# Optimization experiments

Measured on AMD Instinct MI355X. Metric: run time of the kernel, lower is better.

The kernel has to match this reference:

```python
import jax, jax.numpy as jnp
import numpy as np

H = 512   # hidden_size
E = 256   # embedding_size
V = 32000 # vocab_size
L = 1024  # max_length (encoder seq len)
B = 64    # batch


def setup_inputs() -> dict:
    key = jax.random.key(0)
    ks = jax.random.split(key, 18)
    n = lambda i, shape, s=0.05: (jax.random.normal(ks[i], shape, dtype=jnp.float32) * s)
    return {
        "input": jax.random.randint(ks[0], (B, 1), 0, V),
        "last_output_context": n(1, (1, B, H), 1.0),
        "last_hidden": n(2, (1, B, H), 1.0),
        "last_cell_state": n(3, (1, B, H), 1.0),
        "encoder_outputs": n(4, (L, B, H), 1.0),
        "emb": n(5, (V, E)),
        "W_ih": n(6, (4 * H, E + H)),
        "W_hh": n(7, (4 * H, H)),
        "b_ih": n(8, (4 * H,)),
        "b_hh": n(9, (4 * H,)),
        "W_attn": n(10, (H, 2 * H)),
        "b_attn": n(11, (H,)),
        "beta": n(12, (H, 1), 1.0),
        "W_oc": n(13, (H, 2 * H)),
        "b_oc": n(14, (H,)),
        "W_out": n(15, (V, H)),
        "b_out": n(16, (V,)),
    }


def reference(input, last_output_context, last_hidden, last_cell_state,
              encoder_outputs, emb, W_ih, W_hh, b_ih, b_hh,
              W_attn, b_attn, beta, W_oc, b_oc, W_out, b_out):
    # embedding lookup: (B,1) -> (B,E)  (permute(1,0,2) then squeeze step dim)
    tok = emb[input[:, 0]]                                   # (B, E)
    x = jnp.concatenate([tok, last_output_context[0]], axis=1)  # (B, E+H)
    # single-step LSTM (PyTorch gate order i, f, g, o)
    gates = x @ W_ih.T + last_hidden[0] @ W_hh.T + b_ih + b_hh  # (B, 4H)
    i_g, f_g, g_g, o_g = jnp.split(gates, 4, axis=1)
    i_g = jax.nn.sigmoid(i_g)
    f_g = jax.nn.sigmoid(f_g)
    g_g = jnp.tanh(g_g)
    o_g = jax.nn.sigmoid(o_g)
    c = f_g * last_cell_state[0] + i_g * g_g                  # (B, H)
    h = o_g * jnp.tanh(c)                                     # (B, H) == rnn_output
    # additive attention, vectorized over the seq_len loop
    h_tiled = jnp.broadcast_to(h[None], (L, B, H))
    cat = jnp.concatenate([h_tiled, encoder_outputs], axis=-1)  # (L, B, 2H)
    energy = jnp.tanh(cat @ W_attn.T + b_attn) @ beta           # (L, B, 1)
    attn_w = jax.nn.softmax(energy[..., 0], axis=0)             # (L, B) softmax over seq
    # context = bmm(attn_weights, encoder_outputs)
    context = jnp.einsum('lb,lbh->bh', attn_w, encoder_outputs)  # (B, H)
    co = jnp.tanh(jnp.concatenate([h, context], axis=1) @ W_oc.T + b_oc)  # (B, H)
    output = jax.nn.log_softmax(co @ W_out.T + b_out, axis=1)    # (B, V)
    return output, co[None], h[None], c[None]
```

## Files before the change

### kernel.cpp

```cpp
#include <hip/hip_runtime.h>
#include <hip/hip_bf16.h>
#include <cstddef>

#define H   512
#define E   256
#define V   32000
#define L   1024
#define B   64
#define KX  768
#define M_TOT 65536

typedef __attribute__((ext_vector_type(8))) short short8v;
typedef __attribute__((ext_vector_type(4))) float f32x4;

union fu32 { float f; unsigned u; };

__device__ __forceinline__ void split2(float x, unsigned short& h, unsigned short& l) {
    fu32 v; v.f = x;
    h = (unsigned short)(v.u >> 16);
    fu32 hf; hf.u = v.u & 0xFFFF0000u;
    fu32 rv; rv.f = x - hf.f;
    l = (unsigned short)(rv.u >> 16);
}

__global__ __launch_bounds__(256) void k_split_w(const float* __restrict__ W_attn,
                                                 unsigned short* __restrict__ Wh,
                                                 unsigned short* __restrict__ Wl) {
    int e0 = blockIdx.x * 2048 + threadIdx.x * 8;
    int j = e0 >> 9, k = e0 & 511;
    const float* src = &W_attn[(size_t)j * (2 * H) + H + k];
    float4 x0 = *reinterpret_cast<const float4*>(src);
    float4 x1 = *reinterpret_cast<const float4*>(src + 4);
    float xs[8] = {x0.x, x0.y, x0.z, x0.w, x1.x, x1.y, x1.z, x1.w};
    union { short8v v; unsigned short u[8]; } hi, lo;
    #pragma unroll
    for (int i = 0; i < 8; ++i) split2(xs[i], hi.u[i], lo.u[i]);
    *reinterpret_cast<short8v*>(&Wh[e0]) = hi.v;
    *reinterpret_cast<short8v*>(&Wl[e0]) = lo.v;
}

__global__ __launch_bounds__(256) void k_build(const int* __restrict__ inp,
                                               const float* __restrict__ loc,
                                               const float* __restrict__ hprev,
                                               const float* __restrict__ emb,
                                               float* __restrict__ xprevT) {
    int gid = blockIdx.x * 256 + threadIdx.x;
    int k = gid >> 6, b = gid & 63;
    float v;
    if (k < 256)      v = emb[(size_t)inp[b] * E + k];
    else if (k < 768) v = loc[b * H + (k - 256)];
    else              v = hprev[b * H + (k - 768)];
    xprevT[gid] = v;
}

__global__ __launch_bounds__(256) void k_lstm(const float* __restrict__ W_ih,
                                              const float* __restrict__ W_hh,
                                              const float* __restrict__ b_ih,
                                              const float* __restrict__ b_hh,
                                              const float* __restrict__ xprevT,
                                              const float* __restrict__ cprev,
                                              float* __restrict__ h_out,
                                              float* __restrict__ c_out,
                                              float* __restrict__ hnewT) {
    int u = blockIdx.x;
    int w = threadIdx.x >> 6;
    int b = threadIdx.x & 63;
    int j = w * 512 + u;
    float a0 = 0.f, a1 = 0.f, a2 = 0.f, a3 = 0.f;
    const float* Wr = &W_ih[(size_t)j * KX];
    for (int k = 0; k < KX; k += 4) {
        float4 wv = *reinterpret_cast<const float4*>(&Wr[k]);
        a0 += wv.x * xprevT[(k + 0) * 64 + b];
        a1 += wv.y * xprevT[(k + 1) * 64 + b];
        a2 += wv.z * xprevT[(k + 2) * 64 + b];
        a3 += wv.w * xprevT[(k + 3) * 64 + b];
    }
    const float* Wr2 = &W_hh[(size_t)j * H];
    const float* hT = &xprevT[KX * 64];
    for (int k = 0; k < H; k += 4) {
        float4 wv = *reinterpret_cast<const float4*>(&Wr2[k]);
        a0 += wv.x * hT[(k + 0) * 64 + b];
        a1 += wv.y * hT[(k + 1) * 64 + b];
        a2 += wv.z * hT[(k + 2) * 64 + b];
        a3 += wv.w * hT[(k + 3) * 64 + b];
    }
    float acc = b_ih[j] + b_hh[j] + ((a0 + a1) + (a2 + a3));
    __shared__ float gs[4][64];
    gs[w][b] = acc;
    __syncthreads();
    if (threadIdx.x < 64) {
        float ig = 1.f / (1.f + __expf(-gs[0][b]));
        float fg = 1.f / (1.f + __expf(-gs[1][b]));
        float gg = tanhf(gs[2][b]);
        float og = 1.f / (1.f + __expf(-gs[3][b]));
        float c = fg * cprev[b * H + u] + ig * gg;
        float h = og * tanhf(c);
        c_out[b * H + u] = c;
        h_out[b * H + u] = h;
        hnewT[u * 64 + b] = h;
    }
}

__global__ __launch_bounds__(256) void k_hw(const float* __restrict__ W_attn,
                                            const float* __restrict__ b_attn,
                                            const float* __restrict__ hT,
                                            float* __restrict__ hW_jb) {
    int j = blockIdx.x * 4 + (threadIdx.x >> 6);
    int b = threadIdx.x & 63;
    float a0 = 0.f, a1 = 0.f, a2 = 0.f, a3 = 0.f;
    const float* Wr = &W_attn[(size_t)j * (2 * H)];
    for (int k = 0; k < H; k += 4) {
        float4 wv = *reinterpret_cast<const float4*>(&Wr[k]);
        a0 += wv.x * hT[(k + 0) * 64 + b];
        a1 += wv.y * hT[(k + 1) * 64 + b];
        a2 += wv.z * hT[(k + 2) * 64 + b];
        a3 += wv.w * hT[(k + 3) * 64 + b];
    }
    hW_jb[j * 64 + b] = b_attn[j] + ((a0 + a1) + (a2 + a3));
}

#define BKE 32
#define PITCH 40

__global__ __launch_bounds__(256, 3) void k_energy_v3(
        const float* __restrict__ enc,
        const unsigned short* __restrict__ Wh,
        const unsigned short* __restrict__ Wl,
        const float* __restrict__ hW,
        const float* __restrict__ beta,
        float* __restrict__ partial_e) {
    __shared__ unsigned short Ah[128 * PITCH];
    __shared__ unsigned short Al[128 * PITCH];
    __shared__ unsigned short Bh[128 * PITCH];
    __shared__ unsigned short Bl[128 * PITCH];
    __shared__ float red[2][128];

    const int tid  = threadIdx.x;
    const int lane = tid & 63;
    const int wave = tid >> 6;
    const int wm = wave >> 1;
    const int wn = wave & 1;
    const int mt = blockIdx.x >> 2;
    const int jt = blockIdx.x & 3;
    const int m0 = mt * 128;
    const int j0 = jt * 128;

    const int srow = tid >> 2;
    const int skc  = tid & 3;

    float4 ra0[2], ra1[2];
    short8v rb_h[2], rb_l[2];
    #pragma unroll
    for (int p = 0; p < 2; ++p) {
        int row = p * 64 + srow;
        const float* asrc = &enc[(size_t)(m0 + row) * H + skc * 8];
        ra0[p] = *reinterpret_cast<const float4*>(asrc);
        ra1[p] = *reinterpret_cast<const float4*>(asrc + 4);
        size_t bo = (size_t)(j0 + row) * H + skc * 8;
        rb_h[p] = *reinterpret_cast<const short8v*>(&Wh[bo]);
        rb_l[p] = *reinterpret_cast<const short8v*>(&Wl[bo]);
    }

    f32x4 acc[4][4];
    #pragma unroll
    for (int i = 0; i < 4; ++i)
        #pragma unroll
        for (int j = 0; j < 4; ++j) acc[i][j] = (f32x4){0.f, 0.f, 0.f, 0.f};

    for (int k0 = 0; k0 < H; k0 += BKE) {
        __syncthreads();
        #pragma unroll
        for (int p = 0; p < 2; ++p) {
            float xs[8] = {ra0[p].x, ra0[p].y, ra0[p].z, ra0[p].w,
                           ra1[p].x, ra1[p].y, ra1[p].z, ra1[p].w};
            union { short8v v; unsigned short u[8]; } hi, lo;
            #pragma unroll
            for (int i = 0; i < 8; ++i) split2(xs[i], hi.u[i], lo.u[i]);
            int off = (p * 64 + srow) * PITCH + skc * 8;
            *reinterpret_cast<short8v*>(&Ah[off]) = hi.v;
            *reinterpret_cast<short8v*>(&Al[off]) = lo.v;
            *reinterpret_cast<short8v*>(&Bh[off]) = rb_h[p];
            *reinterpret_cast<short8v*>(&Bl[off]) = rb_l[p];
        }
        __syncthreads();
        if (k0 + BKE < H) {
            int kn = k0 + BKE;
            #pragma unroll
            for (int p = 0; p < 2; ++p) {
                int row = p * 64 + srow;
                const float* asrc = &enc[(size_t)(m0 + row) * H + kn + skc * 8];
                ra0[p] = *reinterpret_cast<const float4*>(asrc);
                ra1[p] = *reinterpret_cast<const float4*>(asrc + 4);
                size_t bo = (size_t)(j0 + row) * H + kn + skc * 8;
                rb_h[p] = *reinterpret_cast<const short8v*>(&Wh[bo]);
                rb_l[p] = *reinterpret_cast<const short8v*>(&Wl[bo]);
            }
        }
        const int fr = lane & 15;
        const int kb = (lane >> 4) * 8;
        short8v a_h[4], a_l[4], b_h[4], b_l[4];
        #pragma unroll
        for (int mf = 0; mf < 4; ++mf) {
            int off = (wm * 64 + mf * 16 + fr) * PITCH + kb;
            a_h[mf] = *reinterpret_cast<const short8v*>(&Ah[off]);
            a_l[mf] = *reinterpret_cast<const short8v*>(&Al[off]);
        }
        #pragma unroll
        for (int nf = 0; nf < 4; ++nf) {
            int off = (wn * 64 + nf * 16 + fr) * PITCH + kb;
            b_h[nf] = *reinterpret_cast<const short8v*>(&Bh[off]);
            b_l[nf] = *reinterpret_cast<const short8v*>(&Bl[off]);
        }
        #pragma unroll
        for (int mf = 0; mf < 4; ++mf)
            #pragma unroll
            for (int nf = 0; nf < 4; ++nf) {
                acc[mf][nf] = __builtin_amdgcn_mfma_f32_16x16x32_bf16(
                    a_h[mf], b_h[nf], acc[mf][nf], 0, 0, 0);
                acc[mf][nf] = __builtin_amdgcn_mfma_f32_16x16x32_bf16(
                    a_h[mf], b_l[nf], acc[mf][nf], 0, 0, 0);
                acc[mf][nf] = __builtin_amdgcn_mfma_f32_16x16x32_bf16(
                    a_l[mf], b_h[nf], acc[mf][nf], 0, 0, 0);
            }
    }
    float psum[4][4];
    #pragma unroll
    for (int i = 0; i < 4; ++i)
        #pragma unroll
        for (int r = 0; r < 4; ++r) psum[i][r] = 0.f;
    #pragma unroll
    for (int nf = 0; nf < 4; ++nf) {
        int jj = j0 + wn * 64 + nf * 16 + (lane & 15);
        float bet = beta[jj];
        #pragma unroll
        for (int mf = 0; mf < 4; ++mf) {
            int b_base = (wm * 64 + mf * 16 + (lane >> 4) * 4) & 63;
            float4 hw4 = *reinterpret_cast<const float4*>(&hW[jj * 64 + b_base]);
            float hwv[4] = {hw4.x, hw4.y, hw4.z, hw4.w};
            #pragma unroll
            for (int r = 0; r < 4; ++r) {
                float e = acc[mf][nf][r] + hwv[r];
                float ex = __expf(2.f * e);
                psum[mf][r] += bet * (1.f - 2.f / (ex + 1.f));
            }
        }
    }
    #pragma unroll
    for (int mf = 0; mf < 4; ++mf)
        #pragma unroll
        for (int r = 0; r < 4; ++r) {
            float v = psum[mf][r];
            v += __shfl_xor(v, 1);
            v += __shfl_xor(v, 2);
            v += __shfl_xor(v, 4);
            v += __shfl_xor(v, 8);
            psum[mf][r] = v;
        }
    __syncthreads();
    if ((lane & 15) == 0) {
        #pragma unroll
        for (int mf = 0; mf < 4; ++mf)
            #pragma unroll
            for (int r = 0; r < 4; ++r)
                red[wn][wm * 64 + mf * 16 + (lane >> 4) * 4 + r] = psum[mf][r];
    }
    __syncthreads();
    if (tid < 128)
        partial_e[(size_t)jt * M_TOT + m0 + tid] = red[0][tid] + red[1][tid];
}

__global__ __launch_bounds__(256) void k_softmax_l(const float* __restrict__ partial_e,
                                                   float* __restrict__ attn_w) {
    int b = blockIdx.x;
    int tid = threadIdx.x;
    float el[4];
    float m = -1e30f;
    #pragma unroll
    for (int i = 0; i < 4; ++i) {
        int l = i * 256 + tid;
        float e = 0.f;
        #pragma unroll
        for (int nb = 0; nb < 4; ++nb)
            e += partial_e[(size_t)nb * M_TOT + l * 64 + b];
        el[i] = e;
        m = fmaxf(m, e);
    }
    #pragma unroll
    for (int s = 1; s < 64; s <<= 1) m = fmaxf(m, __shfl_xor(m, s));
    __shared__ float redm[4];
    if ((tid & 63) == 0) redm[tid >> 6] = m;
    __syncthreads();
    m = fmaxf(fmaxf(redm[0], redm[1]), fmaxf(redm[2], redm[3]));
    float s = 0.f;
    #pragma unroll
    for (int i = 0; i < 4; ++i) { el[i] = __expf(el[i] - m); s += el[i]; }
    #pragma unroll
    for (int sh = 1; sh < 64; sh <<= 1) s += __shfl_xor(s, sh);
    __shared__ float reds[4];
    if ((tid & 63) == 0) reds[tid >> 6] = s;
    __syncthreads();
    s = reds[0] + reds[1] + reds[2] + reds[3];
    float inv = 1.f / s;
    #pragma unroll
    for (int i = 0; i < 4; ++i)
        attn_w[(i * 256 + tid) * 64 + b] = el[i] * inv;
}

__global__ __launch_bounds__(256) void k_ctx_part(const float* __restrict__ attn_w,
                                                  const float* __restrict__ enc,
                                                  float* __restrict__ ctx_part) {
    int chunk = blockIdx.x, b = blockIdx.y;
    int h = threadIdx.x * 2;
    float2 acc = {0.f, 0.f};
    for (int i = 0; i < 32; ++i) {
        int l = chunk * 32 + i;
        float w = attn_w[l * 64 + b];
        float2 e2 = *reinterpret_cast<const float2*>(
            &enc[((size_t)l * 64 + b) * H + h]);
        acc.x += w * e2.x;
        acc.y += w * e2.y;
    }
    *reinterpret_cast<float2*>(&ctx_part[((size_t)(chunk * 64 + b)) * H + h]) = acc;
}

__global__ __launch_bounds__(256) void k_ctx_reduce(const float* __restrict__ ctx_part,
                                                    float* __restrict__ ctxT) {
    int gid = blockIdx.x * 256 + threadIdx.x;
    int b = gid >> 9, h = gid & 511;
    float s = 0.f;
    for (int c = 0; c < 32; ++c)
        s += ctx_part[((size_t)(c * 64 + b)) * H + h];
    ctxT[h * 64 + b] = s;
}

__global__ __launch_bounds__(256) void k_co(const float* __restrict__ W_oc,
                                            const float* __restrict__ b_oc,
                                            const float* __restrict__ hT,
                                            const float* __restrict__ ctxT,
                                            float* __restrict__ co_out) {
    int j = blockIdx.x * 4 + (threadIdx.x >> 6);
    int b = threadIdx.x & 63;
    float a0 = 0.f, a1 = 0.f, a2 = 0.f, a3 = 0.f;
    const float* Wr = &W_oc[(size_t)j * (2 * H)];
    for (int k = 0; k < H; k += 4) {
        float4 wv = *reinterpret_cast<const float4*>(&Wr[k]);
        a0 += wv.x * hT[(k + 0) * 64 + b];
        a1 += wv.y * hT[(k + 1) * 64 + b];
        a2 += wv.z * hT[(k + 2) * 64 + b];
        a3 += wv.w * hT[(k + 3) * 64 + b];
    }
    const float* Wr2 = Wr + H;
    for (int k = 0; k < H; k += 4) {
        float4 wv = *reinterpret_cast<const float4*>(&Wr2[k]);
        a0 += wv.x * ctxT[(k + 0) * 64 + b];
        a1 += wv.y * ctxT[(k + 1) * 64 + b];
        a2 += wv.z * ctxT[(k + 2) * 64 + b];
        a3 += wv.w * ctxT[(k + 3) * 64 + b];
    }
    co_out[b * H + j] = tanhf(b_oc[j] + ((a0 + a1) + (a2 + a3)));
}

__global__ __launch_bounds__(256) void k_logits_mfma(const float* __restrict__ co,
                                                     const float* __restrict__ W_out,
                                                     const float* __restrict__ b_out,
                                                     float* __restrict__ logits) {
    __shared__ unsigned short Ah[64 * PITCH];
    __shared__ unsigned short Al[64 * PITCH];
    __shared__ unsigned short Bh[64 * PITCH];
    __shared__ unsigned short Bl[64 * PITCH];

    const int tid  = threadIdx.x;
    const int lane = tid & 63;
    const int wave = tid >> 6;
    const int wm = wave >> 1;
    const int wn = wave & 1;
    const int j0 = blockIdx.x * 64;

    const int srow = tid >> 2;
    const int skc  = tid & 3;

    float4 ra0, ra1, rb0, rb1;
    {
        const float* as = &co[(size_t)srow * H + skc * 8];
        ra0 = *reinterpret_cast<const float4*>(as);
        ra1 = *reinterpret_cast<const float4*>(as + 4);
        const float* bs = &W_out[(size_t)(j0 + srow) * H + skc * 8];
        rb0 = *reinterpret_cast<const float4*>(bs);
        rb1 = *reinterpret_cast<const float4*>(bs + 4);
    }

    f32x4 acc[2][2];
    #pragma unroll
    for (int i = 0; i < 2; ++i)
        #pragma unroll
        for (int j = 0; j < 2; ++j) acc[i][j] = (f32x4){0.f, 0.f, 0.f, 0.f};

    for (int k0 = 0; k0 < H; k0 += BKE) {
        __syncthreads();
        {
            float xs[8] = {ra0.x, ra0.y, ra0.z, ra0.w, ra1.x, ra1.y, ra1.z, ra1.w};
            union { short8v v; unsigned short u[8]; } hi, lo;
            #pragma unroll
            for (int i = 0; i < 8; ++i) split2(xs[i], hi.u[i], lo.u[i]);
            int off = srow * PITCH + skc * 8;
            *reinterpret_cast<short8v*>(&Ah[off]) = hi.v;
            *reinterpret_cast<short8v*>(&Al[off]) = lo.v;
            float ys[8] = {rb0.x, rb0.y, rb0.z, rb0.w, rb1.x, rb1.y, rb1.z, rb1.w};
            union { short8v v; unsigned short u[8]; } hib, lob;
            #pragma unroll
            for (int i = 0; i < 8; ++i) split2(ys[i], hib.u[i], lob.u[i]);
            *reinterpret_cast<short8v*>(&Bh[off]) = hib.v;
            *reinterpret_cast<short8v*>(&Bl[off]) = lob.v;
        }
        __syncthreads();
        if (k0 + BKE < H) {
            int kn = k0 + BKE;
            const float* as = &co[(size_t)srow * H + kn + skc * 8];
            ra0 = *reinterpret_cast<const float4*>(as);
            ra1 = *reinterpret_cast<const float4*>(as + 4);
            const float* bs = &W_out[(size_t)(j0 + srow) * H + kn + skc * 8];
            rb0 = *reinterpret_cast<const float4*>(bs);
            rb1 = *reinterpret_cast<const float4*>(bs + 4);
        }
        const int fr = lane & 15;
        const int kb = (lane >> 4) * 8;
        short8v a_h[2], a_l[2], b_h[2], b_l[2];
        #pragma unroll
        for (int mf = 0; mf < 2; ++mf) {
            int off = (wm * 32 + mf * 16 + fr) * PITCH + kb;
            a_h[mf] = *reinterpret_cast<const short8v*>(&Ah[off]);
            a_l[mf] = *reinterpret_cast<const short8v*>(&Al[off]);
        }
        #pragma unroll
        for (int nf = 0; nf < 2; ++nf) {
            int off = (wn * 32 + nf * 16 + fr) * PITCH + kb;
            b_h[nf] = *reinterpret_cast<const short8v*>(&Bh[off]);
            b_l[nf] = *reinterpret_cast<const short8v*>(&Bl[off]);
        }
        #pragma unroll
        for (int mf = 0; mf < 2; ++mf)
            #pragma unroll
            for (int nf = 0; nf < 2; ++nf) {
                acc[mf][nf] = __builtin_amdgcn_mfma_f32_16x16x32_bf16(
                    a_h[mf], b_h[nf], acc[mf][nf], 0, 0, 0);
                acc[mf][nf] = __builtin_amdgcn_mfma_f32_16x16x32_bf16(
                    a_h[mf], b_l[nf], acc[mf][nf], 0, 0, 0);
                acc[mf][nf] = __builtin_amdgcn_mfma_f32_16x16x32_bf16(
                    a_l[mf], b_h[nf], acc[mf][nf], 0, 0, 0);
            }
    }
    #pragma unroll
    for (int nf = 0; nf < 2; ++nf) {
        int j = j0 + wn * 32 + nf * 16 + (lane & 15);
        float bo = b_out[j];
        #pragma unroll
        for (int mf = 0; mf < 2; ++mf) {
            int mbase = wm * 32 + mf * 16 + (lane >> 4) * 4;
            #pragma unroll
            for (int r = 0; r < 4; ++r)
                logits[(size_t)(mbase + r) * V + j] = acc[mf][nf][r] + bo;
        }
    }
}

__global__ __launch_bounds__(1024) void k_logsm(const float* __restrict__ logits,
                                                float* __restrict__ out) {
    int b = blockIdx.x;
    int tid = threadIdx.x;
    const float* row = &logits[(size_t)b * V];
    float m = -1e30f;
    for (int i = tid; i < V; i += 1024) m = fmaxf(m, row[i]);
    #pragma unroll
    for (int s = 1; s < 64; s <<= 1) m = fmaxf(m, __shfl_xor(m, s));
    __shared__ float redm[16];
    if ((tid & 63) == 0) redm[tid >> 6] = m;
    __syncthreads();
    m = redm[0];
    #pragma unroll
    for (int i = 1; i < 16; ++i) m = fmaxf(m, redm[i]);
    float s = 0.f;
    for (int i = tid; i < V; i += 1024) s += __expf(row[i] - m);
    #pragma unroll
    for (int sh = 1; sh < 64; sh <<= 1) s += __shfl_xor(s, sh);
    __shared__ float reds[16];
    if ((tid & 63) == 0) reds[tid >> 6] = s;
    __syncthreads();
    s = reds[0];
    #pragma unroll
    for (int i = 1; i < 16; ++i) s += reds[i];
    float lse = m + __logf(s);
    for (int i = tid; i < V; i += 1024)
        out[(size_t)b * V + i] = row[i] - lse;
}

extern "C" void kernel_launch(void* const* d_in, const int* in_sizes, int n_in,
                              void* d_out, int out_size, void* d_ws, size_t ws_size,
                              hipStream_t stream) {
    const int*   inp    = (const int*)  d_in[0];
    const float* loc    = (const float*)d_in[1];
    const float* hprev  = (const float*)d_in[2];
    const float* cprev  = (const float*)d_in[3];
    const float* enc    = (const float*)d_in[4];
    const float* emb    = (const float*)d_in[5];
    const float* W_ih   = (const float*)d_in[6];
    const float* W_hh   = (const float*)d_in[7];
    const float* b_ih   = (const float*)d_in[8];
    const float* b_hh   = (const float*)d_in[9];
    const float* W_attn = (const float*)d_in[10];
    const float* b_attn = (const float*)d_in[11];
    const float* beta   = (const float*)d_in[12];
    const float* W_oc   = (const float*)d_in[13];
    const float* b_oc   = (const float*)d_in[14];
    const float* W_out  = (const float*)d_in[15];
    const float* b_out  = (const float*)d_in[16];

    float* out = (float*)d_out;
    float* out_co = out + (size_t)B * V;
    float* out_h  = out_co + B * H;
    float* out_c  = out_h  + B * H;

    float* ws = (float*)d_ws;
    float* xprevT = ws;
    float* hnewT  = xprevT + 1280 * 64;
    float* hW     = hnewT  + H * 64;
    float* pe     = hW     + H * 64;
    float* attnw  = pe     + 4 * M_TOT;
    float* ctxp   = attnw  + M_TOT;
    float* ctxT   = ctxp   + 32 * 64 * H;
    float* logits = ctxT   + H * 64;
    float* ws_end = logits + (size_t)B * V;
    unsigned short* Wh = (unsigned short*)ws_end;
    unsigned short* Wl = Wh + H * H;

    k_split_w<<<128, 256, 0, stream>>>(W_attn, Wh, Wl);
    k_build <<<320, 256, 0, stream>>>(inp, loc, hprev, emb, xprevT);
    k_lstm  <<<512, 256, 0, stream>>>(W_ih, W_hh, b_ih, b_hh, xprevT, cprev,
                                      out_h, out_c, hnewT);
    k_hw    <<<128, 256, 0, stream>>>(W_attn, b_attn, hnewT, hW);
    k_energy_v3<<<2048, 256, 0, stream>>>(enc, Wh, Wl, hW, beta, pe);
    k_softmax_l<<<64, 256, 0, stream>>>(pe, attnw);
    k_ctx_part <<<dim3(32, 64), 256, 0, stream>>>(attnw, enc, ctxp);
    k_ctx_reduce<<<128, 256, 0, stream>>>(ctxp, ctxT);
    k_co    <<<128, 256, 0, stream>>>(W_oc, b_oc, hnewT, ctxT, out_co);
    k_logits_mfma<<<500, 256, 0, stream>>>(out_co, W_out, b_out, logits);
    k_logsm <<<64, 1024, 0, stream>>>(logits, out);
}
```

Measured before the change: 288.7 us.

## Switch energy and logits GEMMs to single-pass fp16 MFMA and split log-softmax

Replaces the three-MFMA bf16 hi/lo split emulation of fp32 in the attention-energy and output-logits GEMMs with a single fp16 MFMA per tile. This cuts MFMA work, halves LDS traffic and footprint, and lets the energy kernel target more blocks per CU. The log-softmax becomes a parallel three-stage partial max/sum, combine and vectorized write, and the context kernel switches to float4 loads. The cost is fp16 precision (about 11-bit mantissa, limited range) on the GEMMs, which may loosen accuracy against the fp32 reference.

```diff
diff --git a/kernel.cpp b/kernel.cpp
--- a/kernel.cpp
+++ b/kernel.cpp
@@ -10,33 +10,21 @@
 #define KX  768
 #define M_TOT 65536
 
-typedef __attribute__((ext_vector_type(8))) short short8v;
+typedef __attribute__((ext_vector_type(8))) _Float16 half8v;
 typedef __attribute__((ext_vector_type(4))) float f32x4;
 
-union fu32 { float f; unsigned u; };
-
-__device__ __forceinline__ void split2(float x, unsigned short& h, unsigned short& l) {
-    fu32 v; v.f = x;
-    h = (unsigned short)(v.u >> 16);
-    fu32 hf; hf.u = v.u & 0xFFFF0000u;
-    fu32 rv; rv.f = x - hf.f;
-    l = (unsigned short)(rv.u >> 16);
-}
-
-__global__ __launch_bounds__(256) void k_split_w(const float* __restrict__ W_attn,
-                                                 unsigned short* __restrict__ Wh,
-                                                 unsigned short* __restrict__ Wl) {
+__global__ __launch_bounds__(256) void k_conv_w(const float* __restrict__ W_attn,
+                                                unsigned short* __restrict__ Wf) {
     int e0 = blockIdx.x * 2048 + threadIdx.x * 8;
     int j = e0 >> 9, k = e0 & 511;
     const float* src = &W_attn[(size_t)j * (2 * H) + H + k];
     float4 x0 = *reinterpret_cast<const float4*>(src);
     float4 x1 = *reinterpret_cast<const float4*>(src + 4);
     float xs[8] = {x0.x, x0.y, x0.z, x0.w, x1.x, x1.y, x1.z, x1.w};
-    union { short8v v; unsigned short u[8]; } hi, lo;
-    #pragma unroll
-    for (int i = 0; i < 8; ++i) split2(xs[i], hi.u[i], lo.u[i]);
-    *reinterpret_cast<short8v*>(&Wh[e0]) = hi.v;
-    *reinterpret_cast<short8v*>(&Wl[e0]) = lo.v;
+    union { half8v v; _Float16 u[8]; } hv;
+    #pragma unroll
+    for (int i = 0; i < 8; ++i) hv.u[i] = (_Float16)xs[i];
+    *reinterpret_cast<half8v*>(&Wf[e0]) = hv.v;
 }
 
 __global__ __launch_bounds__(256) void k_build(const int* __restrict__ inp,
@@ -122,17 +110,14 @@
 #define BKE 32
 #define PITCH 40
 
-__global__ __launch_bounds__(256, 3) void k_energy_v3(
+__global__ __launch_bounds__(256, 4) void k_energy_v4(
         const float* __restrict__ enc,
-        const unsigned short* __restrict__ Wh,
-        const unsigned short* __restrict__ Wl,
+        const unsigned short* __restrict__ Wf,
         const float* __restrict__ hW,
         const float* __restrict__ beta,
         float* __restrict__ partial_e) {
     __shared__ unsigned short Ah[128 * PITCH];
-    __shared__ unsigned short Al[128 * PITCH];
     __shared__ unsigned short Bh[128 * PITCH];
-    __shared__ unsigned short Bl[128 * PITCH];
     __shared__ float red[2][128];
 
     const int tid  = threadIdx.x;
@@ -149,16 +134,14 @@
     const int skc  = tid & 3;
 
     float4 ra0[2], ra1[2];
-    short8v rb_h[2], rb_l[2];
+    half8v rb[2];
     #pragma unroll
     for (int p = 0; p < 2; ++p) {
         int row = p * 64 + srow;
         const float* asrc = &enc[(size_t)(m0 + row) * H + skc * 8];
         ra0[p] = *reinterpret_cast<const float4*>(asrc);
         ra1[p] = *reinterpret_cast<const float4*>(asrc + 4);
-        size_t bo = (size_t)(j0 + row) * H + skc * 8;
-        rb_h[p] = *reinterpret_cast<const short8v*>(&Wh[bo]);
-        rb_l[p] = *reinterpret_cast<const short8v*>(&Wl[bo]);
+        rb[p] = *reinterpret_cast<const half8v*>(&Wf[(size_t)(j0 + row) * H + skc * 8]);
     }
 
     f32x4 acc[4][4];
@@ -173,14 +156,12 @@
         for (int p = 0; p < 2; ++p) {
             float xs[8] = {ra0[p].x, ra0[p].y, ra0[p].z, ra0[p].w,
                            ra1[p].x, ra1[p].y, ra1[p].z, ra1[p].w};
-            union { short8v v; unsigned short u[8]; } hi, lo;
-            #pragma unroll
-            for (int i = 0; i < 8; ++i) split2(xs[i], hi.u[i], lo.u[i]);
+            union { half8v v; _Float16 u[8]; } hv;
+            #pragma unroll
+            for (int i = 0; i < 8; ++i) hv.u[i] = (_Float16)xs[i];
             int off = (p * 64 + srow) * PITCH + skc * 8;
-            *reinterpret_cast<short8v*>(&Ah[off]) = hi.v;
-            *reinterpret_cast<short8v*>(&Al[off]) = lo.v;
-            *reinterpret_cast<short8v*>(&Bh[off]) = rb_h[p];
-            *reinterpret_cast<short8v*>(&Bl[off]) = rb_l[p];
+            *reinterpret_cast<half8v*>(&Ah[off]) = hv.v;
+            *reinterpret_cast<half8v*>(&Bh[off]) = rb[p];
         }
         __syncthreads();
         if (k0 + BKE < H) {
@@ -191,37 +172,28 @@
                 const float* asrc = &enc[(size_t)(m0 + row) * H + kn + skc * 8];
                 ra0[p] = *reinterpret_cast<const float4*>(asrc);
                 ra1[p] = *reinterpret_cast<const float4*>(asrc + 4);
-                size_t bo = (size_t)(j0 + row) * H + kn + skc * 8;
-                rb_h[p] = *reinterpret_cast<const short8v*>(&Wh[bo]);
-                rb_l[p] = *reinterpret_cast<const short8v*>(&Wl[bo]);
+                rb[p] = *reinterpret_cast<const half8v*>(&Wf[(size_t)(j0 + row) * H + kn + skc * 8]);
             }
         }
         const int fr = lane & 15;
         const int kb = (lane >> 4) * 8;
-        short8v a_h[4], a_l[4], b_h[4], b_l[4];
+        half8v a_h[4], b_h[4];
         #pragma unroll
         for (int mf = 0; mf < 4; ++mf) {
             int off = (wm * 64 + mf * 16 + fr) * PITCH + kb;
-            a_h[mf] = *reinterpret_cast<const short8v*>(&Ah[off]);
-            a_l[mf] = *reinterpret_cast<const short8v*>(&Al[off]);
+            a_h[mf] = *reinterpret_cast<const half8v*>(&Ah[off]);
         }
         #pragma unroll
         for (int nf = 0; nf < 4; ++nf) {
             int off = (wn * 64 + nf * 16 + fr) * PITCH + kb;
-            b_h[nf] = *reinterpret_cast<const short8v*>(&Bh[off]);
-            b_l[nf] = *reinterpret_cast<const short8v*>(&Bl[off]);
+            b_h[nf] = *reinterpret_cast<const half8v*>(&Bh[off]);
         }
         #pragma unroll
         for (int mf = 0; mf < 4; ++mf)
             #pragma unroll
-            for (int nf = 0; nf < 4; ++nf) {
-                acc[mf][nf] = __builtin_amdgcn_mfma_f32_16x16x32_bf16(
+            for (int nf = 0; nf < 4; ++nf)
+                acc[mf][nf] = __builtin_amdgcn_mfma_f32_16x16x32_f16(
                     a_h[mf], b_h[nf], acc[mf][nf], 0, 0, 0);
-                acc[mf][nf] = __builtin_amdgcn_mfma_f32_16x16x32_bf16(
-                    a_h[mf], b_l[nf], acc[mf][nf], 0, 0, 0);
-                acc[mf][nf] = __builtin_amdgcn_mfma_f32_16x16x32_bf16(
-                    a_l[mf], b_h[nf], acc[mf][nf], 0, 0, 0);
-            }
     }
     float psum[4][4];
     #pragma unroll
@@ -306,21 +278,23 @@
         attn_w[(i * 256 + tid) * 64 + b] = el[i] * inv;
 }
 
-__global__ __launch_bounds__(256) void k_ctx_part(const float* __restrict__ attn_w,
+__global__ __launch_bounds__(128) void k_ctx_part(const float* __restrict__ attn_w,
                                                   const float* __restrict__ enc,
                                                   float* __restrict__ ctx_part) {
     int chunk = blockIdx.x, b = blockIdx.y;
-    int h = threadIdx.x * 2;
-    float2 acc = {0.f, 0.f};
+    int h = threadIdx.x * 4;
+    float4 acc = {0.f, 0.f, 0.f, 0.f};
     for (int i = 0; i < 32; ++i) {
         int l = chunk * 32 + i;
         float w = attn_w[l * 64 + b];
-        float2 e2 = *reinterpret_cast<const float2*>(
+        float4 e4 = *reinterpret_cast<const float4*>(
             &enc[((size_t)l * 64 + b) * H + h]);
-        acc.x += w * e2.x;
-        acc.y += w * e2.y;
-    }
-    *reinterpret_cast<float2*>(&ctx_part[((size_t)(chunk * 64 + b)) * H + h]) = acc;
+        acc.x += w * e4.x;
+        acc.y += w * e4.y;
+        acc.z += w * e4.z;
+        acc.w += w * e4.w;
+    }
+    *reinterpret_cast<float4*>(&ctx_part[((size_t)(chunk * 64 + b)) * H + h]) = acc;
 }
 
 __global__ __launch_bounds__(256) void k_ctx_reduce(const float* __restrict__ ctx_part,
@@ -360,14 +334,12 @@
     co_out[b * H + j] = tanhf(b_oc[j] + ((a0 + a1) + (a2 + a3)));
 }
 
-__global__ __launch_bounds__(256) void k_logits_mfma(const float* __restrict__ co,
-                                                     const float* __restrict__ W_out,
-                                                     const float* __restrict__ b_out,
-                                                     float* __restrict__ logits) {
+__global__ __launch_bounds__(256) void k_logits_v2(const float* __restrict__ co,
+                                                   const float* __restrict__ W_out,
+                                                   const float* __restrict__ b_out,
+                                                   float* __restrict__ logits) {
     __shared__ unsigned short Ah[64 * PITCH];
-    __shared__ unsigned short Al[64 * PITCH];
     __shared__ unsigned short Bh[64 * PITCH];
-    __shared__ unsigned short Bl[64 * PITCH];
 
     const int tid  = threadIdx.x;
     const int lane = tid & 63;
@@ -399,18 +371,16 @@
         __syncthreads();
         {
             float xs[8] = {ra0.x, ra0.y, ra0.z, ra0.w, ra1.x, ra1.y, ra1.z, ra1.w};
-            union { short8v v; unsigned short u[8]; } hi, lo;
-            #pragma unroll
-            for (int i = 0; i < 8; ++i) split2(xs[i], hi.u[i], lo.u[i]);
+            union { half8v v; _Float16 u[8]; } ha;
+            #pragma unroll
+            for (int i = 0; i < 8; ++i) ha.u[i] = (_Float16)xs[i];
+            float ys[8] = {rb0.x, rb0.y, rb0.z, rb0.w, rb1.x, rb1.y, rb1.z, rb1.w};
+            union { half8v v; _Float16 u[8]; } hb;
+            #pragma unroll
+            for (int i = 0; i < 8; ++i) hb.u[i] = (_Float16)ys[i];
             int off = srow * PITCH + skc * 8;
-            *reinterpret_cast<short8v*>(&Ah[off]) = hi.v;
-            *reinterpret_cast<short8v*>(&Al[off]) = lo.v;
-            float ys[8] = {rb0.x, rb0.y, rb0.z, rb0.w, rb1.x, rb1.y, rb1.z, rb1.w};
-            union { short8v v; unsigned short u[8]; } hib, lob;
-            #pragma unroll
-            for (int i = 0; i < 8; ++i) split2(ys[i], hib.u[i], lob.u[i]);
-            *reinterpret_cast<short8v*>(&Bh[off]) = hib.v;
-            *reinterpret_cast<short8v*>(&Bl[off]) = lob.v;
+            *reinterpret_cast<half8v*>(&Ah[off]) = ha.v;
+            *reinterpret_cast<half8v*>(&Bh[off]) = hb.v;
         }
         __syncthreads();
         if (k0 + BKE < H) {
@@ -424,30 +394,23 @@
         }
         const int fr = lane & 15;
         const int kb = (lane >> 4) * 8;
-        short8v a_h[2], a_l[2], b_h[2], b_l[2];
+        half8v a_h[2], b_h[2];
         #pragma unroll
         for (int mf = 0; mf < 2; ++mf) {
             int off = (wm * 32 + mf * 16 + fr) * PITCH + kb;
-            a_h[mf] = *reinterpret_cast<const short8v*>(&Ah[off]);
-            a_l[mf] = *reinterpret_cast<const short8v*>(&Al[off]);
+            a_h[mf] = *reinterpret_cast<const half8v*>(&Ah[off]);
         }
         #pragma unroll
         for (int nf = 0; nf < 2; ++nf) {
             int off = (wn * 32 + nf * 16 + fr) * PITCH + kb;
-            b_h[nf] = *reinterpret_cast<const short8v*>(&Bh[off]);
-            b_l[nf] = *reinterpret_cast<const short8v*>(&Bl[off]);
+            b_h[nf] = *reinterpret_cast<const half8v*>(&Bh[off]);
         }
         #pragma unroll
         for (int mf = 0; mf < 2; ++mf)
             #pragma unroll
-            for (int nf = 0; nf < 2; ++nf) {
-                acc[mf][nf] = __builtin_amdgcn_mfma_f32_16x16x32_bf16(
+            for (int nf = 0; nf < 2; ++nf)
+                acc[mf][nf] = __builtin_amdgcn_mfma_f32_16x16x32_f16(
                     a_h[mf], b_h[nf], acc[mf][nf], 0, 0, 0);
-                acc[mf][nf] = __builtin_amdgcn_mfma_f32_16x16x32_bf16(
-                    a_h[mf], b_l[nf], acc[mf][nf], 0, 0, 0);
-                acc[mf][nf] = __builtin_amdgcn_mfma_f32_16x16x32_bf16(
-                    a_l[mf], b_h[nf], acc[mf][nf], 0, 0, 0);
-            }
     }
     #pragma unroll
     for (int nf = 0; nf < 2; ++nf) {
@@ -463,34 +426,62 @@
     }
 }
 
-__global__ __launch_bounds__(1024) void k_logsm(const float* __restrict__ logits,
-                                                float* __restrict__ out) {
-    int b = blockIdx.x;
+__global__ __launch_bounds__(256) void k_lsm_part(const float* __restrict__ logits,
+                                                  float* __restrict__ pmax,
+                                                  float* __restrict__ psum) {
+    int chunk = blockIdx.x, b = blockIdx.y;
     int tid = threadIdx.x;
-    const float* row = &logits[(size_t)b * V];
+    const float* row = &logits[(size_t)b * V + chunk * 4000];
+    float v[16];
     float m = -1e30f;
-    for (int i = tid; i < V; i += 1024) m = fmaxf(m, row[i]);
+    #pragma unroll
+    for (int t = 0; t < 16; ++t) {
+        int i = t * 256 + tid;
+        v[t] = (i < 4000) ? row[i] : -1e30f;
+        m = fmaxf(m, v[t]);
+    }
     #pragma unroll
     for (int s = 1; s < 64; s <<= 1) m = fmaxf(m, __shfl_xor(m, s));
-    __shared__ float redm[16];
+    __shared__ float redm[4];
     if ((tid & 63) == 0) redm[tid >> 6] = m;
     __syncthreads();
-    m = redm[0];
-    #pragma unroll
-    for (int i = 1; i < 16; ++i) m = fmaxf(m, redm[i]);
+    m = fmaxf(fmaxf(redm[0], redm[1]), fmaxf(redm[2], redm[3]));
     float s = 0.f;
-    for (int i = tid; i < V; i += 1024) s += __expf(row[i] - m);
+    #pragma unroll
+    for (int t = 0; t < 16; ++t) s += __expf(v[t] - m);
     #pragma unroll
     for (int sh = 1; sh < 64; sh <<= 1) s += __shfl_xor(s, sh);
-    __shared__ float reds[16];
+    __shared__ float reds[4];
     if ((tid & 63) == 0) reds[tid >> 6] = s;
     __syncthreads();
-    s = reds[0];
-    #pragma unroll
-    for (int i = 1; i < 16; ++i) s += reds[i];
-    float lse = m + __logf(s);
-    for (int i = tid; i < V; i += 1024)
-        out[(size_t)b * V + i] = row[i] - lse;
+    if (tid == 0) {
+        pmax[chunk * 64 + b] = m;
+        psum[chunk * 64 + b] = reds[0] + reds[1] + reds[2] + reds[3];
+    }
+}
+
+__global__ __launch_bounds__(64) void k_lsm_final(const float* __restrict__ pmax,
+                                                  const float* __restrict__ psum,
+                                                  float* __restrict__ lse) {
+    int b = threadIdx.x;
+    float m = -1e30f;
+    #pragma unroll
+    for (int c = 0; c < 8; ++c) m = fmaxf(m, pmax[c * 64 + b]);
+    float s = 0.f;
+    #pragma unroll
+    for (int c = 0; c < 8; ++c) s += psum[c * 64 + b] * __expf(pmax[c * 64 + b] - m);
+    lse[b] = m + __logf(s);
+}
+
+__global__ __launch_bounds__(256) void k_lsm_write(const float* __restrict__ logits,
+                                                   const float* __restrict__ lse,
+                                                   float* __restrict__ out) {
+    size_t i4 = ((size_t)blockIdx.x * 256 + threadIdx.x) * 4;
+    int b = (int)(i4 / V);
+    float l = lse[b];
+    float4 x = *reinterpret_cast<const float4*>(&logits[i4]);
+    x.x -= l; x.y -= l; x.z -= l; x.w -= l;
+    *reinterpret_cast<float4*>(&out[i4]) = x;
 }
 
 extern "C" void kernel_launch(void* const* d_in, const int* in_sizes, int n_in,
@@ -528,20 +519,23 @@
     float* ctxp   = attnw  + M_TOT;
     float* ctxT   = ctxp   + 32 * 64 * H;
     float* logits = ctxT   + H * 64;
-    float* ws_end = logits + (size_t)B * V;
-    unsigned short* Wh = (unsigned short*)ws_end;
-    unsigned short* Wl = Wh + H * H;
-
-    k_split_w<<<128, 256, 0, stream>>>(W_attn, Wh, Wl);
+    float* pmax   = logits + (size_t)B * V;
+    float* psum   = pmax   + 512;
+    float* lse    = psum   + 512;
+    unsigned short* Wf = (unsigned short*)(lse + 64);
+
+    k_conv_w<<<128, 256, 0, stream>>>(W_attn, Wf);
     k_build <<<320, 256, 0, stream>>>(inp, loc, hprev, emb, xprevT);
     k_lstm  <<<512, 256, 0, stream>>>(W_ih, W_hh, b_ih, b_hh, xprevT, cprev,
                                       out_h, out_c, hnewT);
     k_hw    <<<128, 256, 0, stream>>>(W_attn, b_attn, hnewT, hW);
-    k_energy_v3<<<2048, 256, 0, stream>>>(enc, Wh, Wl, hW, beta, pe);
+    k_energy_v4<<<2048, 256, 0, stream>>>(enc, Wf, hW, beta, pe);
     k_softmax_l<<<64, 256, 0, stream>>>(pe, attnw);
-    k_ctx_part <<<dim3(32, 64), 256, 0, stream>>>(attnw, enc, ctxp);
+    k_ctx_part <<<dim3(32, 64), 128, 0, stream>>>(attnw, enc, ctxp);
     k_ctx_reduce<<<128, 256, 0, stream>>>(ctxp, ctxT);
     k_co    <<<128, 256, 0, stream>>>(W_oc, b_oc, hnewT, ctxT, out_co);
-    k_logits_mfma<<<500, 256, 0, stream>>>(out_co, W_out, b_out, logits);
-    k_logsm <<<64, 1024, 0, stream>>>(logits, out);
-}
+    k_logits_v2<<<500, 256, 0, stream>>>(out_co, W_out, b_out, logits);
+    k_lsm_part<<<dim3(8, 64), 256, 0, stream>>>(logits, pmax, psum);
+    k_lsm_final<<<1, 64, 0, stream>>>(pmax, psum, lse);
+    k_lsm_write<<<2000, 256, 0, stream>>>(logits, lse, out);
+}
```

Result: faster. 257.1 us (-10.9%).
